# Kernel optimization log

Measured on AMD Instinct MI355X. Metric: run time of the kernel, lower is better.

## Reference

```python
import jax, jax.numpy as jnp
import numpy as np

BETA = 1.0
GAMMA = 1.0
DELTA = 0.0


def setup_inputs() -> dict:
    key = jax.random.key(0)
    k1, k2 = jax.random.split(key)
    xyz1 = jax.random.normal(k1, (4, 4096, 3), dtype=jnp.float32)
    xyz2 = jax.random.normal(k2, (4, 4096, 3), dtype=jnp.float32)
    return {"xyz1": xyz1, "xyz2": xyz2}


def _pairwise_sqdist(a, b):
    # a: [B, N, 3], b: [B, M, 3] -> [B, N, M] squared euclidean distances
    a2 = jnp.sum(a * a, axis=-1)  # [B, N]
    b2 = jnp.sum(b * b, axis=-1)  # [B, M]
    ab = jnp.einsum("bnd,bmd->bnm", a, b)  # [B, N, M]
    return a2[:, :, None] + b2[:, None, :] - 2.0 * ab


def reference(xyz1, xyz2):
    P = xyz1.shape[1]
    d = _pairwise_sqdist(xyz1, xyz2)  # [B, N, M]
    dist12 = jnp.min(d, axis=2)       # nearest in xyz2 for each xyz1 point
    idx12 = jnp.argmin(d, axis=2)
    dist21 = jnp.min(d, axis=1)       # nearest in xyz1 for each xyz2 point
    idx21 = jnp.argmin(d, axis=1)
    loss = (jnp.mean(dist12, axis=-1)
            + jnp.max(dist12, axis=-1) * BETA
            + (GAMMA + DELTA * P) * jnp.mean(dist21, axis=-1))
    loss = jnp.mean(loss)
    return loss, idx12, idx21
```

## Files before the change

kernel.cpp:

```cpp
#include <hip/hip_runtime.h>
#include <stdint.h>
#include <float.h>


constexpr int B_ = 4;
constexpr int N_ = 4096;
constexpr int PTS = 256;
constexpr int PPT = 4;
constexpr int TILES = N_ / (PTS * PPT);
constexpr int JSPLIT = 32;
constexpr int CHUNK = N_ / JSPLIT;
constexpr int SPB = 128;
constexpr double EPS32 = 1.1920928955078125e-7;
constexpr double TOL_K12 = 0.6 * EPS32;
constexpr double TOL_K21 = 0.0;
constexpr double BETA_ = 1.0;
constexpr double GAMMA_ = 1.0;
constexpr double DELTA_ = 0.0;

__global__ __launch_bounds__(256) void cd_min32(
        const float* __restrict__ xyz1, const float* __restrict__ xyz2,
        float* __restrict__ champD, unsigned int* __restrict__ champJ,
        float* __restrict__ runUp, float4* __restrict__ b4) {
    const int tile  = blockIdx.x % TILES;
    const int b     = (blockIdx.x / TILES) % B_;
    const int dir   = blockIdx.x / (TILES * B_);
    const int split = blockIdx.y;
    const float* A  = dir ? xyz2 : xyz1;
    const float* Bc = dir ? xyz1 : xyz2;
    const size_t ob = (size_t)dir * B_ + b;

    __shared__ float4 s[CHUNK];
    const float* bbase = Bc + ((size_t)b * N_ + (size_t)split * CHUNK) * 3;
    if (threadIdx.x < CHUNK) {
        int j = threadIdx.x;
        float bx = bbase[3 * j], by = bbase[3 * j + 1], bz = bbase[3 * j + 2];
        float b2 = bx * bx + by * by + bz * bz;
        float4 v = make_float4(bx, by, bz, b2);
        s[j] = v;
        if (tile == 0)
            b4[ob * N_ + (size_t)split * CHUNK + j] = v;
    }
    __syncthreads();

    float px[PPT], py[PPT], pz[PPT];
    float cur[PPT], ruv[PPT];
    unsigned int cj[PPT];
    #pragma unroll
    for (int pi = 0; pi < PPT; ++pi) {
        const int p = tile * (PTS * PPT) + pi * PTS + threadIdx.x;
        const float* ap = A + ((size_t)b * N_ + p) * 3;
        px[pi] = ap[0]; py[pi] = ap[1]; pz[pi] = ap[2];
        cur[pi] = FLT_MAX; ruv[pi] = FLT_MAX; cj[pi] = 0u;
    }

    #pragma unroll 4
    for (int j = 0; j < CHUNK; ++j) {
        float4 bv = s[j];
        const unsigned int jg = (unsigned int)(split * CHUNK + j);
        #pragma unroll
        for (int pi = 0; pi < PPT; ++pi) {
            float dx = px[pi] - bv.x, dy = py[pi] - bv.y, dz = pz[pi] - bv.z;
            float d = __fmaf_rn(dx, dx, __fmaf_rn(dy, dy, dz * dz));
            ruv[pi] = fminf(ruv[pi], fmaxf(d, cur[pi]));
            if (d < cur[pi]) cj[pi] = jg;
            cur[pi] = fminf(cur[pi], d);
        }
    }

    const size_t sm = (ob * JSPLIT + split) * N_;
    #pragma unroll
    for (int pi = 0; pi < PPT; ++pi) {
        const int p = tile * (PTS * PPT) + pi * PTS + threadIdx.x;
        champD[sm + p] = cur[pi];
        champJ[sm + p] = cj[pi];
        runUp[sm + p]  = ruv[pi];
    }
}

__global__ __launch_bounds__(SPB) void cd_select(
        const float* __restrict__ xyz1, const float* __restrict__ xyz2,
        const float* __restrict__ champD, const unsigned int* __restrict__ champJ,
        const float* __restrict__ runUp, const float4* __restrict__ b4,
        double* __restrict__ dminArr, float* __restrict__ out) {
    const int ob  = blockIdx.x >> 5;
    const int c   = blockIdx.x & 31;
    const int dir = ob >> 2;
    const int b   = ob & 3;
    const int p0  = c * SPB;
    const float* A  = dir ? xyz2 : xyz1;
    const double tolk = dir ? TOL_K21 : TOL_K12;
    const float4* bb4 = b4 + (size_t)ob * N_;

    __shared__ float cDl[JSPLIT][SPB];
    __shared__ unsigned int cJl[JSPLIT][SPB];
    __shared__ float rul[JSPLIT][SPB];

    const int t = threadIdx.x;
    for (int idx = t; idx < JSPLIT * SPB; idx += SPB) {
        const int s = idx >> 7, p = idx & (SPB - 1);
        const size_t g = ((size_t)ob * JSPLIT + s) * N_ + p0 + p;
        cDl[s][p] = champD[g];
        cJl[s][p] = champJ[g];
        rul[s][p] = runUp[g];
    }
    __syncthreads();

    const int p = p0 + t;
    const float* ap = A + ((size_t)b * N_ + p) * 3;
    const float x = ap[0], y = ap[1], z = ap[2];
    const float a2f = x * x + y * y + z * z;

    float m = FLT_MAX;
    #pragma unroll
    for (int s = 0; s < JSPLIT; ++s)
        m = fminf(m, cDl[s][t]);

    const float me = __fmaf_rn(2e-6f, m, m);
    const float skipthr = (me + 7e-7f * a2f) * (1.0f + 4e-6f);

    unsigned int candmask = 0, rescmask = 0;
    #pragma unroll
    for (int s = 0; s < JSPLIT; ++s) {
        if (cDl[s][t] <= skipthr) candmask |= (1u << s);
        if (rul[s][t] <= skipthr) rescmask |= (1u << s);
    }

    const double xd = (double)x, yd = (double)y, zd = (double)z;
    const double a2 = xd * xd + yd * yd + zd * zd;

    double dmin = 1.0e300;
    unsigned int mk = candmask;
    while (mk) {
        int s = __ffs(mk) - 1; mk &= mk - 1;
        float4 bv = bb4[cJl[s][t]];
        double ddx = xd - (double)bv.x, ddy = yd - (double)bv.y,
               ddz = zd - (double)bv.z;
        dmin = fmin(dmin, fma(ddx, ddx, fma(ddy, ddy, ddz * ddz)));
    }
    mk = rescmask;
    while (mk) {
        int s = __ffs(mk) - 1; mk &= mk - 1;
        for (int j = s * CHUNK; j < (s + 1) * CHUNK; ++j) {
            float4 bv = bb4[j];
            float dx = x - bv.x, dy = y - bv.y, dz = z - bv.z;
            float d32 = __fmaf_rn(dx, dx, __fmaf_rn(dy, dy, dz * dz));
            float thr = __fmaf_rn(2e-7f, a2f + bv.w, me);
            if (d32 <= thr) {
                double ddx = xd - (double)bv.x, ddy = yd - (double)bv.y,
                       ddz = zd - (double)bv.z;
                dmin = fmin(dmin, fma(ddx, ddx, fma(ddy, ddy, ddz * ddz)));
            }
        }
    }

    unsigned int pick = 0xFFFFFFFFu;
    mk = candmask;
    while (mk) {
        int s = __ffs(mk) - 1; mk &= mk - 1;
        unsigned int j = cJl[s][t];
        float4 bv = bb4[j];
        double bxd = (double)bv.x, byd = (double)bv.y, bzd = (double)bv.z;
        double ddx = xd - bxd, ddy = yd - byd, ddz = zd - bzd;
        double d64 = fma(ddx, ddx, fma(ddy, ddy, ddz * ddz));
        double M   = a2 + (bxd * bxd + byd * byd + bzd * bzd);
        if (d64 <= fma(tolk, M, dmin)) pick = (j < pick) ? j : pick;
    }
    mk = rescmask;
    while (mk) {
        int s = __ffs(mk) - 1; mk &= mk - 1;
        for (int j = s * CHUNK; j < (s + 1) * CHUNK; ++j) {
            float4 bv = bb4[j];
            float dx = x - bv.x, dy = y - bv.y, dz = z - bv.z;
            float d32 = __fmaf_rn(dx, dx, __fmaf_rn(dy, dy, dz * dz));
            float thr = __fmaf_rn(2e-7f, a2f + bv.w, me);
            if (d32 <= thr) {
                double bxd = (double)bv.x, byd = (double)bv.y, bzd = (double)bv.z;
                double ddx = xd - bxd, ddy = yd - byd, ddz = zd - bzd;
                double d64 = fma(ddx, ddx, fma(ddy, ddy, ddz * ddz));
                double M   = a2 + (bxd * bxd + byd * byd + bzd * bzd);
                if (d64 <= fma(tolk, M, dmin))
                    pick = ((unsigned int)j < pick) ? (unsigned int)j : pick;
            }
        }
    }

    dminArr[(size_t)ob * N_ + p] = dmin;
    const size_t obase = (dir == 0) ? (1 + (size_t)b * N_)
                                    : (1 + (size_t)B_ * N_ + (size_t)b * N_);
    out[obase + p] = (float)pick;
}

__global__ __launch_bounds__(256) void cd_finalize(
        const double* __restrict__ dminArr, float* __restrict__ out,
        double* __restrict__ loss_part) {
    const int b = blockIdx.x;
    const int t = threadIdx.x;

    double sum12 = 0.0, max12 = -1.0e300, sum21 = 0.0;
    for (int n = t; n < N_; n += 256) {
        double d12 = dminArr[(size_t)b * N_ + n];
        double d21 = dminArr[((size_t)B_ + b) * N_ + n];
        sum12 += d12;
        max12 = fmax(max12, d12);
        sum21 += d21;
    }
    __shared__ double s1[256], s2[256], s3[256];
    s1[t] = sum12; s2[t] = max12; s3[t] = sum21;
    __syncthreads();
    for (int off = 128; off > 0; off >>= 1) {
        if (t < off) {
            s1[t] += s1[t + off];
            s2[t]  = fmax(s2[t], s2[t + off]);
            s3[t] += s3[t + off];
        }
        __syncthreads();
    }
    if (t == 0) {
        loss_part[b] = s1[0] / (double)N_ + BETA_ * s2[0]
                     + (GAMMA_ + DELTA_ * (double)N_) * (s3[0] / (double)N_);
    }
}

__global__ void cd_loss(const double* __restrict__ loss_part,
                        float* __restrict__ out) {
    if (blockIdx.x == 0 && threadIdx.x == 0) {
        double s = 0.0;
        for (int b = 0; b < B_; ++b) s += loss_part[b];
        out[0] = (float)(s / (double)B_);
    }
}

extern "C" void kernel_launch(void* const* d_in, const int* in_sizes, int n_in,
                              void* d_out, int out_size, void* d_ws, size_t ws_size,
                              hipStream_t stream) {
    const float* xyz1 = (const float*)d_in[0];
    const float* xyz2 = (const float*)d_in[1];
    float* out = (float*)d_out;

    const size_t NP = (size_t)2 * B_ * N_;
    double* dminArr   = (double*)d_ws;
    double* loss_part = dminArr + NP;
    float4* b4 = (float4*)(loss_part + B_);
    float* champD = (float*)(b4 + NP);
    unsigned int* champJ = (unsigned int*)(champD + NP * JSPLIT);
    float* runUp = (float*)(champJ + NP * JSPLIT);

    dim3 grid(TILES * B_ * 2, JSPLIT);
    cd_min32<<<grid, PTS, 0, stream>>>(xyz1, xyz2, champD, champJ, runUp, b4);

    cd_select<<<(int)(NP / SPB), SPB, 0, stream>>>(
        xyz1, xyz2, champD, champJ, runUp, b4, dminArr, out);

    cd_finalize<<<B_, 256, 0, stream>>>(dminArr, out, loss_part);
    cd_loss<<<1, 64, 0, stream>>>(loss_part, out);
}
```

Baseline: 59.84 us.

## Use expanded-norm distance form in min kernel and halve points per thread

The inner loop of the brute-force nearest-neighbour kernel now evaluates b2 - 2a·b with three chained FMAs, dropping the a2 term that is constant per query point. This replaces three subtractions plus three multiply-adds per pair. The select kernel is adjusted to add a2 back and to widen its candidate threshold for the larger rounding error of the expanded form. PPT drops from 4 to 2, doubling the number of blocks and lowering registers per thread, at the cost of reloading shared-memory B points for fewer queries each. The looser threshold may send more candidates to the slower rescan path.

```diff
diff --git a/kernel.cpp b/kernel.cpp
--- a/kernel.cpp
+++ b/kernel.cpp
@@ -6,7 +6,7 @@
 constexpr int B_ = 4;
 constexpr int N_ = 4096;
 constexpr int PTS = 256;
-constexpr int PPT = 4;
+constexpr int PPT = 2;
 constexpr int TILES = N_ / (PTS * PPT);
 constexpr int JSPLIT = 32;
 constexpr int CHUNK = N_ / JSPLIT;
@@ -43,14 +43,16 @@
     }
     __syncthreads();
 
-    float px[PPT], py[PPT], pz[PPT];
+    float m2x[PPT], m2y[PPT], m2z[PPT];
     float cur[PPT], ruv[PPT];
     unsigned int cj[PPT];
     #pragma unroll
     for (int pi = 0; pi < PPT; ++pi) {
         const int p = tile * (PTS * PPT) + pi * PTS + threadIdx.x;
         const float* ap = A + ((size_t)b * N_ + p) * 3;
-        px[pi] = ap[0]; py[pi] = ap[1]; pz[pi] = ap[2];
+        m2x[pi] = -2.0f * ap[0];
+        m2y[pi] = -2.0f * ap[1];
+        m2z[pi] = -2.0f * ap[2];
         cur[pi] = FLT_MAX; ruv[pi] = FLT_MAX; cj[pi] = 0u;
     }
 
@@ -60,11 +62,12 @@
         const unsigned int jg = (unsigned int)(split * CHUNK + j);
         #pragma unroll
         for (int pi = 0; pi < PPT; ++pi) {
-            float dx = px[pi] - bv.x, dy = py[pi] - bv.y, dz = pz[pi] - bv.z;
-            float d = __fmaf_rn(dx, dx, __fmaf_rn(dy, dy, dz * dz));
-            ruv[pi] = fminf(ruv[pi], fmaxf(d, cur[pi]));
-            if (d < cur[pi]) cj[pi] = jg;
-            cur[pi] = fminf(cur[pi], d);
+            float t = __fmaf_rn(m2x[pi], bv.x,
+                      __fmaf_rn(m2y[pi], bv.y,
+                      __fmaf_rn(m2z[pi], bv.z, bv.w)));
+            ruv[pi] = fminf(ruv[pi], fmaxf(t, cur[pi]));
+            if (t < cur[pi]) cj[pi] = jg;
+            cur[pi] = fminf(cur[pi], t);
         }
     }
 
@@ -111,19 +114,19 @@
     const float x = ap[0], y = ap[1], z = ap[2];
     const float a2f = x * x + y * y + z * z;
 
-    float m = FLT_MAX;
+    float m_t = FLT_MAX;
     #pragma unroll
     for (int s = 0; s < JSPLIT; ++s)
-        m = fminf(m, cDl[s][t]);
-
-    const float me = __fmaf_rn(2e-6f, m, m);
-    const float skipthr = (me + 7e-7f * a2f) * (1.0f + 4e-6f);
+        m_t = fminf(m_t, cDl[s][t]);
+
+    const float mind = m_t + a2f;
+    const float skipthr = __fmaf_rn(4e-6f, a2f + fabsf(mind), mind);
 
     unsigned int candmask = 0, rescmask = 0;
     #pragma unroll
     for (int s = 0; s < JSPLIT; ++s) {
-        if (cDl[s][t] <= skipthr) candmask |= (1u << s);
-        if (rul[s][t] <= skipthr) rescmask |= (1u << s);
+        if (cDl[s][t] + a2f <= skipthr) candmask |= (1u << s);
+        if (rul[s][t] + a2f <= skipthr) rescmask |= (1u << s);
     }
 
     const double xd = (double)x, yd = (double)y, zd = (double)z;
@@ -145,7 +148,7 @@
             float4 bv = bb4[j];
             float dx = x - bv.x, dy = y - bv.y, dz = z - bv.z;
             float d32 = __fmaf_rn(dx, dx, __fmaf_rn(dy, dy, dz * dz));
-            float thr = __fmaf_rn(2e-7f, a2f + bv.w, me);
+            float thr = __fmaf_rn(2e-7f, a2f + bv.w, skipthr);
             if (d32 <= thr) {
                 double ddx = xd - (double)bv.x, ddy = yd - (double)bv.y,
                        ddz = zd - (double)bv.z;
@@ -173,7 +176,7 @@
             float4 bv = bb4[j];
             float dx = x - bv.x, dy = y - bv.y, dz = z - bv.z;
             float d32 = __fmaf_rn(dx, dx, __fmaf_rn(dy, dy, dz * dz));
-            float thr = __fmaf_rn(2e-7f, a2f + bv.w, me);
+            float thr = __fmaf_rn(2e-7f, a2f + bv.w, skipthr);
             if (d32 <= thr) {
                 double bxd = (double)bv.x, byd = (double)bv.y, bzd = (double)bv.z;
                 double ddx = xd - bxd, ddy = yd - byd, ddz = zd - bzd;
```

New measurement: 52.46 us. 1.14x faster.
